# Kernel optimization log

Hardware: AMD Instinct MI355X
Metric: run time of the kernel (lower is better)

## Reference

```python
import jax, jax.numpy as jnp
import numpy as np

EPS = 1e-5

def _layernorm(x, g, b):
    m = jnp.mean(x, axis=-1, keepdims=True)
    v = jnp.mean(jnp.square(x - m), axis=-1, keepdims=True)
    return (x - m) * jax.lax.rsqrt(v + EPS) * g + b

def setup_inputs() -> dict:
    key = jax.random.key(0)
    ks = jax.random.split(key, 4)
    B, N, D = 8, 256, 128
    h = jax.random.normal(ks[0], (B, N, D), dtype=jnp.float32)
    adj_J = jax.random.normal(ks[1], (B, N, N), dtype=jnp.float32)
    W_msg = jax.random.normal(ks[2], (D, 2 * D + 1), dtype=jnp.float32) * 0.05
    W_upd = jax.random.normal(ks[3], (D, 2 * D), dtype=jnp.float32) * 0.05
    return {
        "h": h, "adj_J": adj_J,
        "W_msg": W_msg, "b_msg": jnp.zeros((D,), jnp.float32),
        "g_msg": jnp.ones((D,), jnp.float32), "beta_msg": jnp.zeros((D,), jnp.float32),
        "W_upd": W_upd, "b_upd": jnp.zeros((D,), jnp.float32),
        "g_upd": jnp.ones((D,), jnp.float32), "beta_upd": jnp.zeros((D,), jnp.float32),
    }

def reference(h, adj_J, W_msg, b_msg, g_msg, beta_msg, W_upd, b_upd, g_upd, beta_upd):
    B, N, D = h.shape
    # Split msg Linear weight: cat([h_target, h_source, J]) @ W.T is separable.
    Wt = W_msg[:, :D]        # acts on h_target (node i, dim 1)
    Ws = W_msg[:, D:2 * D]   # acts on h_source (node j, dim 2)
    wJ = W_msg[:, 2 * D]     # acts on scalar J
    # pre[b,i,j,e] = h[b,i]@Wt.T + h[b,j]@Ws.T + J[b,i,j]*wJ + b
    pre = (jnp.einsum('bid,ed->bie', h, Wt)[:, :, None, :]
           + jnp.einsum('bjd,ed->bje', h, Ws)[:, None, :, :]
           + adj_J[..., None] * wJ
           + b_msg)
    messages = jax.nn.silu(_layernorm(pre, g_msg, beta_msg))  # (B,N,N,D)
    # mask out self-messages (j == i) then sum over sources j
    idx = jnp.arange(N)
    agg = jnp.sum(messages, axis=2) - messages[:, idx, idx, :]  # (B,N,D)
    upd_pre = (jnp.einsum('bnd,ed->bne', h, W_upd[:, :D])
               + jnp.einsum('bnd,ed->bne', agg, W_upd[:, D:])
               + b_upd)
    dh = jax.nn.silu(_layernorm(upd_pre, g_upd, beta_upd))
    return h + dh
```

## Files before the change

kernel.cpp:

```cpp
#include <hip/hip_runtime.h>

#define BB 8
#define NN 256
#define DD 128
#define SW 257
#define SU 256
#define EPSV 1e-5f

__device__ __forceinline__ float wave_reduce_add(float v) {
#pragma unroll
  for (int off = 32; off > 0; off >>= 1) v += __shfl_xor(v, off, 64);
  return v;
}

__global__ __launch_bounds__(256) void k_proj(
    const float* __restrict__ h, const float* __restrict__ Wm,
    const float* __restrict__ bmsg,
    float* __restrict__ u, float* __restrict__ s,
    float* __restrict__ rowA, float* __restrict__ rowB,
    float* __restrict__ rowD2, float* __restrict__ rowE2,
    float* __restrict__ wtilv) {
  const int blk = blockIdx.x;
  const int b = blk >> 6;
  const int r0 = (blk & 63) * 4;
  const int tid = threadIdx.x;
  const int half = tid >> 7, e = tid & 127;
  const int wv = tid >> 6, lane = tid & 63;

  __shared__ float hs[4][DD];
  __shared__ float pS[4][4], pw[2], pQ[4][4], pD[4][4];

  const float* hb = h + (size_t)(b * NN + r0) * DD;
  if (tid < DD) {
#pragma unroll
    for (int r = 0; r < 4; ++r) hs[r][e] = hb[r * DD + e];
  }
  __syncthreads();

  float acc[4];
  const float bm = (half == 0) ? bmsg[e] : 0.f;
#pragma unroll
  for (int r = 0; r < 4; ++r) acc[r] = bm;

  const float* wr = Wm + (size_t)e * SW + half * DD;
#pragma unroll 8
  for (int k = 0; k < DD; k += 4) {
    const float4 w4 = *(const float4*)(wr + k);
#pragma unroll
    for (int r = 0; r < 4; ++r) {
      const float4 hv = *(const float4*)(&hs[r][k]);
      acc[r] = fmaf(hv.x, w4.x, acc[r]);
      acc[r] = fmaf(hv.y, w4.y, acc[r]);
      acc[r] = fmaf(hv.z, w4.z, acc[r]);
      acc[r] = fmaf(hv.w, w4.w, acc[r]);
    }
  }

  const float we = Wm[(size_t)e * SW + 2 * DD];
#pragma unroll
  for (int r = 0; r < 4; ++r) {
    const float sm = wave_reduce_add(acc[r]);
    if (lane == 0) pS[wv][r] = sm;
  }
  {
    const float sw = wave_reduce_add(we);
    if (lane == 0 && wv < 2) pw[wv] = sw;
  }
  __syncthreads();

  const int b2 = half * 2;
  const float muw = (pw[0] + pw[1]) * (1.f / DD);
  const float wtil = we - muw;
  float c[4];
#pragma unroll
  for (int r = 0; r < 4; ++r)
    c[r] = acc[r] - (pS[b2][r] + pS[b2 + 1][r]) * (1.f / DD);

  float* outp = (half == 0 ? u : s) + (size_t)(b * NN + r0) * DD;
#pragma unroll
  for (int r = 0; r < 4; ++r) outp[r * DD + e] = c[r];
  if (blk == 0 && half == 0) wtilv[e] = wtil;

#pragma unroll
  for (int r = 0; r < 4; ++r) {
    const float q = wave_reduce_add(c[r] * c[r]);
    const float dd = wave_reduce_add(c[r] * wtil);
    if (lane == 0) { pQ[wv][r] = q; pD[wv][r] = dd; }
  }
  __syncthreads();
  if (tid < 4) {
    const int row = b * NN + r0 + tid;
    rowA[row]  = pQ[0][tid] + pQ[1][tid];
    rowD2[row] = 2.f * (pD[0][tid] + pD[1][tid]);
    rowB[row]  = pQ[2][tid] + pQ[3][tid];
    rowE2[row] = 2.f * (pD[2][tid] + pD[3][tid]);
  }
}

__global__ __launch_bounds__(256) void k_cross(
    const float* __restrict__ u, const float* __restrict__ s,
    const float* __restrict__ rowA, const float* __restrict__ rowB,
    float* __restrict__ Gp) {
  const int bid = blockIdx.x;
  const int b = bid >> 6;
  const int t = bid & 63;
  const int r0 = (t >> 3) * 32, c0 = (t & 7) * 32;
  const int tid = threadIdx.x;
  const int ty = tid >> 4, tx = tid & 15;

  __shared__ float Us[32][132], Ss[32][132];
  const float* ub = u + (size_t)(b * NN + r0) * DD;
  const float* sb = s + (size_t)(b * NN + c0) * DD;
  {
    const int row = tid >> 5, col = (tid & 31) * 4;
#pragma unroll
    for (int rr = 0; rr < 4; ++rr) {
      const float4 uv = *(const float4*)(ub + (size_t)(row + rr * 8) * DD + col);
      const float4 sv = *(const float4*)(sb + (size_t)(row + rr * 8) * DD + col);
      *(float4*)(&Us[row + rr * 8][col]) = uv;
      *(float4*)(&Ss[row + rr * 8][col]) = sv;
    }
  }
  __syncthreads();

  float a00 = 0, a01 = 0, a10 = 0, a11 = 0;
  for (int k = 0; k < DD; k += 4) {
    const float4 A0 = *(const float4*)(&Us[ty][k]);
    const float4 A1 = *(const float4*)(&Us[ty + 16][k]);
    const float4 B0 = *(const float4*)(&Ss[tx][k]);
    const float4 B1 = *(const float4*)(&Ss[tx + 16][k]);
    a00 = fmaf(A0.x, B0.x, a00); a00 = fmaf(A0.y, B0.y, a00);
    a00 = fmaf(A0.z, B0.z, a00); a00 = fmaf(A0.w, B0.w, a00);
    a01 = fmaf(A0.x, B1.x, a01); a01 = fmaf(A0.y, B1.y, a01);
    a01 = fmaf(A0.z, B1.z, a01); a01 = fmaf(A0.w, B1.w, a01);
    a10 = fmaf(A1.x, B0.x, a10); a10 = fmaf(A1.y, B0.y, a10);
    a10 = fmaf(A1.z, B0.z, a10); a10 = fmaf(A1.w, B0.w, a10);
    a11 = fmaf(A1.x, B1.x, a11); a11 = fmaf(A1.y, B1.y, a11);
    a11 = fmaf(A1.z, B1.z, a11); a11 = fmaf(A1.w, B1.w, a11);
  }
  const float Ar0 = rowA[b * NN + r0 + ty];
  const float Ar1 = rowA[b * NN + r0 + ty + 16];
  const float Bc0 = rowB[b * NN + c0 + tx];
  const float Bc1 = rowB[b * NN + c0 + tx + 16];
  float* gp = Gp + ((size_t)(b * NN + r0 + ty)) * NN + c0;
  gp[tx]                = Ar0 + Bc0 + 2.f * a00;
  gp[tx + 16]           = Ar0 + Bc1 + 2.f * a01;
  gp[16 * NN + tx]      = Ar1 + Bc0 + 2.f * a10;
  gp[16 * NN + tx + 16] = Ar1 + Bc1 + 2.f * a11;
}

__global__ __launch_bounds__(256) void k_msg(
    const float* __restrict__ u, const float* __restrict__ s,
    const float* __restrict__ Gp, const float* __restrict__ rowD2,
    const float* __restrict__ rowE2, const float* __restrict__ adj,
    const float* __restrict__ wtilv, const float* __restrict__ g,
    const float* __restrict__ be, float* __restrict__ agg) {
  const int blk = blockIdx.x;
  const int b = blk >> 8, i = blk & 255;
  const int tid = threadIdx.x, lane = tid & 63, wv = tid >> 6;

  __shared__ float4 s_pak[NN];
  __shared__ float sacc[4][DD];

  s_pak[tid] = make_float4(adj[(size_t)blk * NN + tid],
                           Gp[(size_t)blk * NN + tid],
                           rowE2[b * NN + tid], 0.f);

  const float2 uu  = *(const float2*)(u + (size_t)blk * DD + 2 * lane);
  const float2 wt2 = *(const float2*)(wtilv + 2 * lane);
  const float2 g2  = *(const float2*)(g + 2 * lane);
  const float2 be2 = *(const float2*)(be + 2 * lane);
  const float C = wave_reduce_add(fmaf(wt2.x, wt2.x, wt2.y * wt2.y));
  const float D2i = rowD2[blk];
  __syncthreads();

  float acc0 = 0.f, acc1 = 0.f;
  const float* srow = s + (size_t)b * NN * DD + 2 * lane;
#pragma unroll 4
  for (int j = wv; j < NN; j += 4) {
    if (j == i) continue;
    const float4 pk = s_pak[j];
    const float2 ss = *(const float2*)(srow + (size_t)j * DD);
    const float aJ = pk.x;
    const float q = fmaf(aJ, fmaf(aJ, C, D2i + pk.z), pk.y);
    const float rs = __builtin_amdgcn_rsqf(fmaf(q, 1.f / DD, EPSV));
    const float x0 = fmaf(aJ, wt2.x, uu.x + ss.x);
    const float x1 = fmaf(aJ, wt2.y, uu.y + ss.y);
    const float y0 = fmaf(x0 * rs, g2.x, be2.x);
    const float y1 = fmaf(x1 * rs, g2.y, be2.y);
    acc0 = fmaf(y0, __builtin_amdgcn_rcpf(1.f + __expf(-y0)), acc0);
    acc1 = fmaf(y1, __builtin_amdgcn_rcpf(1.f + __expf(-y1)), acc1);
  }
  *(float2*)(&sacc[wv][2 * lane]) = make_float2(acc0, acc1);
  __syncthreads();
  if (tid < DD) {
    agg[(size_t)blk * DD + tid] =
        sacc[0][tid] + sacc[1][tid] + sacc[2][tid] + sacc[3][tid];
  }
}

__global__ __launch_bounds__(256) void k_upd(
    const float* __restrict__ h, const float* __restrict__ agg,
    const float* __restrict__ Wu, const float* __restrict__ bu,
    const float* __restrict__ gu, const float* __restrict__ beu,
    float* __restrict__ out) {
  const int blk = blockIdx.x;
  const int b = blk >> 6;
  const int r0 = (blk & 63) * 4;
  const int tid = threadIdx.x;
  const int half = tid >> 7, e = tid & 127;
  const int wv = tid >> 6, lane = tid & 63;

  __shared__ float hs[4][DD], ags[4][DD], comb[4][DD];
  __shared__ float pm[2][4], pq[2][4];
  const size_t base = (size_t)(b * NN + r0) * DD;
  if (tid < DD) {
#pragma unroll
    for (int r = 0; r < 4; ++r) hs[r][e] = h[base + r * DD + e];
  } else {
#pragma unroll
    for (int r = 0; r < 4; ++r) ags[r][e] = agg[base + r * DD + e];
  }
  __syncthreads();

  float acc[4];
  const float bias = (half == 0) ? bu[e] : 0.f;
#pragma unroll
  for (int r = 0; r < 4; ++r) acc[r] = bias;

  const float* wr = Wu + (size_t)e * SU + half * DD;
  const float(*inp)[DD] = (half == 0) ? hs : ags;
#pragma unroll 8
  for (int k = 0; k < DD; k += 4) {
    const float4 w4 = *(const float4*)(wr + k);
#pragma unroll
    for (int r = 0; r < 4; ++r) {
      const float4 hv = *(const float4*)(&inp[r][k]);
      acc[r] = fmaf(hv.x, w4.x, acc[r]);
      acc[r] = fmaf(hv.y, w4.y, acc[r]);
      acc[r] = fmaf(hv.z, w4.z, acc[r]);
      acc[r] = fmaf(hv.w, w4.w, acc[r]);
    }
  }
  if (half == 1) {
#pragma unroll
    for (int r = 0; r < 4; ++r) comb[r][e] = acc[r];
  }
  __syncthreads();
  float v[4];
  if (half == 0) {
#pragma unroll
    for (int r = 0; r < 4; ++r) {
      v[r] = acc[r] + comb[r][e];
      const float sm = wave_reduce_add(v[r]);
      const float sq = wave_reduce_add(v[r] * v[r]);
      if (lane == 0) { pm[wv][r] = sm; pq[wv][r] = sq; }
    }
  }
  __syncthreads();
  if (half == 0) {
    const float ge = gu[e], bee = beu[e];
#pragma unroll
    for (int r = 0; r < 4; ++r) {
      const float mean = (pm[0][r] + pm[1][r]) * (1.f / DD);
      const float var = (pq[0][r] + pq[1][r]) * (1.f / DD) - mean * mean;
      const float rs = __builtin_amdgcn_rsqf(var + EPSV);
      const float y = fmaf((v[r] - mean) * rs, ge, bee);
      const float sg = __builtin_amdgcn_rcpf(1.f + __expf(-y));
      out[base + r * DD + e] = hs[r][e] + y * sg;
    }
  }
}

extern "C" void kernel_launch(void* const* d_in, const int* in_sizes, int n_in,
                              void* d_out, int out_size, void* d_ws, size_t ws_size,
                              hipStream_t stream) {
  const float* h    = (const float*)d_in[0];
  const float* adj  = (const float*)d_in[1];
  const float* Wm   = (const float*)d_in[2];
  const float* bmsg = (const float*)d_in[3];
  const float* gmsg = (const float*)d_in[4];
  const float* bemsg= (const float*)d_in[5];
  const float* Wu   = (const float*)d_in[6];
  const float* bupd = (const float*)d_in[7];
  const float* gupd = (const float*)d_in[8];
  const float* beupd= (const float*)d_in[9];
  float* out = (float*)d_out;

  float* ws    = (float*)d_ws;
  float* u     = ws;
  float* s     = u + BB * NN * DD;
  float* aggp  = s + BB * NN * DD;
  float* Gp    = aggp + BB * NN * DD;
  float* rowA  = Gp + BB * NN * NN;
  float* rowB  = rowA + BB * NN;
  float* rowD2 = rowB + BB * NN;
  float* rowE2 = rowD2 + BB * NN;
  float* wtilv = rowE2 + BB * NN;

  k_proj<<<512, 256, 0, stream>>>(h, Wm, bmsg, u, s, rowA, rowB, rowD2, rowE2, wtilv);
  k_cross<<<512, 256, 0, stream>>>(u, s, rowA, rowB, Gp);
  k_msg<<<2048, 256, 0, stream>>>(u, s, Gp, rowD2, rowE2, adj, wtilv, gmsg, bemsg, aggp);
  k_upd<<<512, 256, 0, stream>>>(h, aggp, Wu, bupd, gupd, beupd, out);
}
```

Before: 65.46 us.

## Fuse four stage kernels into one cooperative persistent kernel with grid syncs

Replaces the four separate launches (projection, cross Gram, message aggregation, update) with a single cooperative kernel of 1024 blocks that runs each stage in turn, separated by grid-wide syncs. The message stage now has each block handle two rows instead of one row per block. The aim is to remove the launch gaps and tail effects between the four kernels. In exchange it adds three grid barriers and leaves half the blocks idle during three of the stages. It falls back to the old four-kernel path if the occupancy check or the cooperative launch fails.

```diff
diff --git a/kernel.cpp b/kernel.cpp
--- a/kernel.cpp
+++ b/kernel.cpp
@@ -1,4 +1,7 @@
 #include <hip/hip_runtime.h>
+#include <hip/hip_cooperative_groups.h>
+
+namespace cg = cooperative_groups;
 
 #define BB 8
 #define NN 256
@@ -6,11 +9,266 @@
 #define SW 257
 #define SU 256
 #define EPSV 1e-5f
+#define NBF 1024
 
 __device__ __forceinline__ float wave_reduce_add(float v) {
 #pragma unroll
   for (int off = 32; off > 0; off >>= 1) v += __shfl_xor(v, off, 64);
   return v;
+}
+
+__global__ __launch_bounds__(256, 4) void k_fused(
+    const float* __restrict__ h, const float* __restrict__ adj,
+    const float* __restrict__ Wm, const float* __restrict__ bmsg,
+    const float* __restrict__ g, const float* __restrict__ be,
+    const float* __restrict__ Wu, const float* __restrict__ bu,
+    const float* __restrict__ gu, const float* __restrict__ beu,
+    float* __restrict__ out,
+    float* __restrict__ u, float* __restrict__ s, float* __restrict__ aggp,
+    float* __restrict__ Gp, float* __restrict__ rowA, float* __restrict__ rowB,
+    float* __restrict__ rowD2, float* __restrict__ rowE2,
+    float* __restrict__ wtilv) {
+  cg::grid_group grid = cg::this_grid();
+  const int blk = blockIdx.x;
+  const int tid = threadIdx.x;
+  const int lane = tid & 63, wv = tid >> 6;
+
+  __shared__ __align__(16) float smem[2 * 32 * 132];
+  __shared__ float ps_a[4][4], ps_b[4][4], ps_c[4][4], ps_w[2];
+
+  if (blk < 512) {
+    const int b = blk >> 6, r0 = (blk & 63) * 4;
+    const int half = tid >> 7, e = tid & 127;
+    float (*hs)[DD] = (float (*)[DD])smem;
+    const float* hb = h + (size_t)(b * NN + r0) * DD;
+    if (tid < DD) {
+#pragma unroll
+      for (int r = 0; r < 4; ++r) hs[r][e] = hb[r * DD + e];
+    }
+    __syncthreads();
+
+    float acc[4];
+    const float bm = (half == 0) ? bmsg[e] : 0.f;
+#pragma unroll
+    for (int r = 0; r < 4; ++r) acc[r] = bm;
+
+    const float* wr = Wm + (size_t)e * SW + half * DD;
+#pragma unroll 8
+    for (int k = 0; k < DD; k += 4) {
+      const float4 w4 = *(const float4*)(wr + k);
+#pragma unroll
+      for (int r = 0; r < 4; ++r) {
+        const float4 hv = *(const float4*)(&hs[r][k]);
+        acc[r] = fmaf(hv.x, w4.x, acc[r]);
+        acc[r] = fmaf(hv.y, w4.y, acc[r]);
+        acc[r] = fmaf(hv.z, w4.z, acc[r]);
+        acc[r] = fmaf(hv.w, w4.w, acc[r]);
+      }
+    }
+
+    const float we = Wm[(size_t)e * SW + 2 * DD];
+#pragma unroll
+    for (int r = 0; r < 4; ++r) {
+      const float sm = wave_reduce_add(acc[r]);
+      if (lane == 0) ps_a[wv][r] = sm;
+    }
+    {
+      const float sw = wave_reduce_add(we);
+      if (lane == 0 && wv < 2) ps_w[wv] = sw;
+    }
+    __syncthreads();
+
+    const int b2 = half * 2;
+    const float muw = (ps_w[0] + ps_w[1]) * (1.f / DD);
+    const float wtil = we - muw;
+    float c[4];
+#pragma unroll
+    for (int r = 0; r < 4; ++r)
+      c[r] = acc[r] - (ps_a[b2][r] + ps_a[b2 + 1][r]) * (1.f / DD);
+
+    float* outp = (half == 0 ? u : s) + (size_t)(b * NN + r0) * DD;
+#pragma unroll
+    for (int r = 0; r < 4; ++r) outp[r * DD + e] = c[r];
+    if (blk == 0 && half == 0) wtilv[e] = wtil;
+
+#pragma unroll
+    for (int r = 0; r < 4; ++r) {
+      const float q = wave_reduce_add(c[r] * c[r]);
+      const float dd = wave_reduce_add(c[r] * wtil);
+      if (lane == 0) { ps_b[wv][r] = q; ps_c[wv][r] = dd; }
+    }
+    __syncthreads();
+    if (tid < 4) {
+      const int row = b * NN + r0 + tid;
+      rowA[row]  = ps_b[0][tid] + ps_b[1][tid];
+      rowD2[row] = 2.f * (ps_c[0][tid] + ps_c[1][tid]);
+      rowB[row]  = ps_b[2][tid] + ps_b[3][tid];
+      rowE2[row] = 2.f * (ps_c[2][tid] + ps_c[3][tid]);
+    }
+  }
+  grid.sync();
+
+  if (blk < 512) {
+    const int b = blk >> 6;
+    const int t = blk & 63;
+    const int r0 = (t >> 3) * 32, c0 = (t & 7) * 32;
+    const int ty = tid >> 4, tx = tid & 15;
+    float (*Us)[132] = (float (*)[132])smem;
+    float (*Ss)[132] = (float (*)[132])(smem + 32 * 132);
+    const float* ub = u + (size_t)(b * NN + r0) * DD;
+    const float* sb = s + (size_t)(b * NN + c0) * DD;
+    {
+      const int row = tid >> 5, col = (tid & 31) * 4;
+#pragma unroll
+      for (int rr = 0; rr < 4; ++rr) {
+        const float4 uv = *(const float4*)(ub + (size_t)(row + rr * 8) * DD + col);
+        const float4 sv = *(const float4*)(sb + (size_t)(row + rr * 8) * DD + col);
+        *(float4*)(&Us[row + rr * 8][col]) = uv;
+        *(float4*)(&Ss[row + rr * 8][col]) = sv;
+      }
+    }
+    __syncthreads();
+
+    float a00 = 0, a01 = 0, a10 = 0, a11 = 0;
+    for (int k = 0; k < DD; k += 4) {
+      const float4 A0 = *(const float4*)(&Us[ty][k]);
+      const float4 A1 = *(const float4*)(&Us[ty + 16][k]);
+      const float4 B0 = *(const float4*)(&Ss[tx][k]);
+      const float4 B1 = *(const float4*)(&Ss[tx + 16][k]);
+      a00 = fmaf(A0.x, B0.x, a00); a00 = fmaf(A0.y, B0.y, a00);
+      a00 = fmaf(A0.z, B0.z, a00); a00 = fmaf(A0.w, B0.w, a00);
+      a01 = fmaf(A0.x, B1.x, a01); a01 = fmaf(A0.y, B1.y, a01);
+      a01 = fmaf(A0.z, B1.z, a01); a01 = fmaf(A0.w, B1.w, a01);
+      a10 = fmaf(A1.x, B0.x, a10); a10 = fmaf(A1.y, B0.y, a10);
+      a10 = fmaf(A1.z, B0.z, a10); a10 = fmaf(A1.w, B0.w, a10);
+      a11 = fmaf(A1.x, B1.x, a11); a11 = fmaf(A1.y, B1.y, a11);
+      a11 = fmaf(A1.z, B1.z, a11); a11 = fmaf(A1.w, B1.w, a11);
+    }
+    const float Ar0 = rowA[b * NN + r0 + ty];
+    const float Ar1 = rowA[b * NN + r0 + ty + 16];
+    const float Bc0 = rowB[b * NN + c0 + tx];
+    const float Bc1 = rowB[b * NN + c0 + tx + 16];
+    float* gp = Gp + ((size_t)(b * NN + r0 + ty)) * NN + c0;
+    gp[tx]                = Ar0 + Bc0 + 2.f * a00;
+    gp[tx + 16]           = Ar0 + Bc1 + 2.f * a01;
+    gp[16 * NN + tx]      = Ar1 + Bc0 + 2.f * a10;
+    gp[16 * NN + tx + 16] = Ar1 + Bc1 + 2.f * a11;
+  }
+  grid.sync();
+
+  {
+    float4* s_pak = (float4*)smem;
+    float (*sacc)[DD] = (float (*)[DD])(smem + 1024);
+
+    const float2 wt2 = *(const float2*)(wtilv + 2 * lane);
+    const float2 g2  = *(const float2*)(g + 2 * lane);
+    const float2 be2 = *(const float2*)(be + 2 * lane);
+    const float C = wave_reduce_add(fmaf(wt2.x, wt2.x, wt2.y * wt2.y));
+
+#pragma unroll
+    for (int it = 0; it < 2; ++it) {
+      const int idx = blk + it * NBF;
+      const int b = idx >> 8, i = idx & 255;
+
+      s_pak[tid] = make_float4(adj[(size_t)idx * NN + tid],
+                               Gp[(size_t)idx * NN + tid],
+                               rowE2[b * NN + tid], 0.f);
+      const float2 uu = *(const float2*)(u + (size_t)idx * DD + 2 * lane);
+      const float D2i = rowD2[idx];
+      __syncthreads();
+
+      float acc0 = 0.f, acc1 = 0.f;
+      const float* srow = s + (size_t)b * NN * DD + 2 * lane;
+#pragma unroll 4
+      for (int j = wv; j < NN; j += 4) {
+        if (j == i) continue;
+        const float4 pk = s_pak[j];
+        const float2 ss = *(const float2*)(srow + (size_t)j * DD);
+        const float aJ = pk.x;
+        const float q = fmaf(aJ, fmaf(aJ, C, D2i + pk.z), pk.y);
+        const float rs = __builtin_amdgcn_rsqf(fmaf(q, 1.f / DD, EPSV));
+        const float x0 = fmaf(aJ, wt2.x, uu.x + ss.x);
+        const float x1 = fmaf(aJ, wt2.y, uu.y + ss.y);
+        const float y0 = fmaf(x0 * rs, g2.x, be2.x);
+        const float y1 = fmaf(x1 * rs, g2.y, be2.y);
+        acc0 = fmaf(y0, __builtin_amdgcn_rcpf(1.f + __expf(-y0)), acc0);
+        acc1 = fmaf(y1, __builtin_amdgcn_rcpf(1.f + __expf(-y1)), acc1);
+      }
+      *(float2*)(&sacc[wv][2 * lane]) = make_float2(acc0, acc1);
+      __syncthreads();
+      if (tid < DD) {
+        aggp[(size_t)idx * DD + tid] =
+            sacc[0][tid] + sacc[1][tid] + sacc[2][tid] + sacc[3][tid];
+      }
+      __syncthreads();
+    }
+  }
+  grid.sync();
+
+  if (blk < 512) {
+    const int b = blk >> 6, r0 = (blk & 63) * 4;
+    const int half = tid >> 7, e = tid & 127;
+    float (*hs)[DD]   = (float (*)[DD])smem;
+    float (*ags)[DD]  = (float (*)[DD])(smem + 512);
+    float (*comb)[DD] = (float (*)[DD])(smem + 1024);
+    const size_t base = (size_t)(b * NN + r0) * DD;
+    if (tid < DD) {
+#pragma unroll
+      for (int r = 0; r < 4; ++r) hs[r][e] = h[base + r * DD + e];
+    } else {
+#pragma unroll
+      for (int r = 0; r < 4; ++r) ags[r][e] = aggp[base + r * DD + e];
+    }
+    __syncthreads();
+
+    float acc[4];
+    const float bias = (half == 0) ? bu[e] : 0.f;
+#pragma unroll
+    for (int r = 0; r < 4; ++r) acc[r] = bias;
+
+    const float* wr = Wu + (size_t)e * SU + half * DD;
+    const float(*inp)[DD] = (half == 0) ? hs : ags;
+#pragma unroll 8
+    for (int k = 0; k < DD; k += 4) {
+      const float4 w4 = *(const float4*)(wr + k);
+#pragma unroll
+      for (int r = 0; r < 4; ++r) {
+        const float4 hv = *(const float4*)(&inp[r][k]);
+        acc[r] = fmaf(hv.x, w4.x, acc[r]);
+        acc[r] = fmaf(hv.y, w4.y, acc[r]);
+        acc[r] = fmaf(hv.z, w4.z, acc[r]);
+        acc[r] = fmaf(hv.w, w4.w, acc[r]);
+      }
+    }
+    if (half == 1) {
+#pragma unroll
+      for (int r = 0; r < 4; ++r) comb[r][e] = acc[r];
+    }
+    __syncthreads();
+    float v[4];
+    if (half == 0) {
+#pragma unroll
+      for (int r = 0; r < 4; ++r) {
+        v[r] = acc[r] + comb[r][e];
+        const float sm = wave_reduce_add(v[r]);
+        const float sq = wave_reduce_add(v[r] * v[r]);
+        if (lane == 0) { ps_a[wv][r] = sm; ps_b[wv][r] = sq; }
+      }
+    }
+    __syncthreads();
+    if (half == 0) {
+      const float ge = gu[e], bee = beu[e];
+#pragma unroll
+      for (int r = 0; r < 4; ++r) {
+        const float mean = (ps_a[0][r] + ps_a[1][r]) * (1.f / DD);
+        const float var = (ps_b[0][r] + ps_b[1][r]) * (1.f / DD) - mean * mean;
+        const float rs = __builtin_amdgcn_rsqf(var + EPSV);
+        const float y = fmaf((v[r] - mean) * rs, ge, bee);
+        const float sg = __builtin_amdgcn_rcpf(1.f + __expf(-y));
+        out[base + r * DD + e] = hs[r][e] + y * sg;
+      }
+    }
+  }
 }
 
 __global__ __launch_bounds__(256) void k_proj(
@@ -298,6 +556,21 @@
   float* rowE2 = rowD2 + BB * NN;
   float* wtilv = rowE2 + BB * NN;
 
+  int maxBlocksPerCU = 0;
+  hipError_t qe = hipOccupancyMaxActiveBlocksPerMultiprocessor(
+      &maxBlocksPerCU, (const void*)k_fused, 256, 0);
+  if (qe == hipSuccess && maxBlocksPerCU >= 4) {
+    void* args[] = {(void*)&h,    (void*)&adj,  (void*)&Wm,    (void*)&bmsg,
+                    (void*)&gmsg, (void*)&bemsg,(void*)&Wu,    (void*)&bupd,
+                    (void*)&gupd, (void*)&beupd,(void*)&out,   (void*)&u,
+                    (void*)&s,    (void*)&aggp, (void*)&Gp,    (void*)&rowA,
+                    (void*)&rowB, (void*)&rowD2,(void*)&rowE2, (void*)&wtilv};
+    hipError_t le = hipLaunchCooperativeKernel((const void*)k_fused,
+                                               dim3(NBF), dim3(256), args, 0,
+                                               stream);
+    if (le == hipSuccess) return;
+  }
+
   k_proj<<<512, 256, 0, stream>>>(h, Wm, bmsg, u, s, rowA, rowB, rowD2, rowE2, wtilv);
   k_cross<<<512, 256, 0, stream>>>(u, s, rowA, rowB, Gp);
   k_msg<<<2048, 256, 0, stream>>>(u, s, Gp, rowD2, rowE2, adj, wtilv, gmsg, bemsg, aggp);
```

Result: no change. 66.28 us (+1.3%).

## Fuse cross-term, message aggregation and update into one kernel over row pairs

Applied to the files above, without the earlier changes.

Replaces the k_cross, k_msg and k_upd kernels with a single kernel that handles two target rows per block. It tiles s through shared memory, computes the u·s dot products on the fly instead of materializing the Gp matrix, aggregates messages, and then applies the update linear, layernorm and SiLU in place. k_proj now also writes a transposed copy of W_upd so the fused update reads weights coalesced. This removes two kernel launches and the global round trips for Gp and agg, but each block now reloads all of s for only two rows and has less parallelism per block.

```diff
diff --git a/kernel.cpp b/kernel.cpp
--- a/kernel.cpp
+++ b/kernel.cpp
@@ -15,11 +15,11 @@
 
 __global__ __launch_bounds__(256) void k_proj(
     const float* __restrict__ h, const float* __restrict__ Wm,
-    const float* __restrict__ bmsg,
+    const float* __restrict__ bmsg, const float* __restrict__ Wu,
     float* __restrict__ u, float* __restrict__ s,
     float* __restrict__ rowA, float* __restrict__ rowB,
     float* __restrict__ rowD2, float* __restrict__ rowE2,
-    float* __restrict__ wtilv) {
+    float* __restrict__ wtilv, float* __restrict__ wut) {
   const int blk = blockIdx.x;
   const int b = blk >> 6;
   const int r0 = (blk & 63) * 4;
@@ -35,6 +35,11 @@
 #pragma unroll
     for (int r = 0; r < 4; ++r) hs[r][e] = hb[r * DD + e];
   }
+  if (tid >= DD && tid < DD + 64) {
+    const int i = blk * 64 + (tid - DD);
+    const int d = i >> 7, e2 = i & 127;
+    wut[i] = Wu[(size_t)e2 * SU + d];
+  }
   __syncthreads();
 
   float acc[4];
@@ -97,177 +102,170 @@
   }
 }
 
-__global__ __launch_bounds__(256) void k_cross(
-    const float* __restrict__ u, const float* __restrict__ s,
+__global__ __launch_bounds__(256) void k_msgfused(
+    const float* __restrict__ h, const float* __restrict__ u,
+    const float* __restrict__ s, const float* __restrict__ adj,
     const float* __restrict__ rowA, const float* __restrict__ rowB,
-    float* __restrict__ Gp) {
-  const int bid = blockIdx.x;
-  const int b = bid >> 6;
-  const int t = bid & 63;
-  const int r0 = (t >> 3) * 32, c0 = (t & 7) * 32;
-  const int tid = threadIdx.x;
-  const int ty = tid >> 4, tx = tid & 15;
-
-  __shared__ float Us[32][132], Ss[32][132];
-  const float* ub = u + (size_t)(b * NN + r0) * DD;
-  const float* sb = s + (size_t)(b * NN + c0) * DD;
+    const float* __restrict__ rowD2, const float* __restrict__ rowE2,
+    const float* __restrict__ wtilv, const float* __restrict__ g,
+    const float* __restrict__ be, const float* __restrict__ wut,
+    const float* __restrict__ bu, const float* __restrict__ gu,
+    const float* __restrict__ beu, float* __restrict__ out) {
+  const int blk = blockIdx.x;
+  const int b = blk >> 7, ip = blk & 127;
+  const int i0 = 2 * ip, i1 = i0 + 1;
+  const int tid = threadIdx.x, lane = tid & 63, wv = tid >> 6;
+  const int bNN = b * NN;
+
+  __shared__ __align__(16) float st_[32 * 132];
+  __shared__ __align__(16) float upair_[2 * DD];
+  __shared__ __align__(16) float hrow_[2 * DD];
+  __shared__ float2 pak0[32], pak1[32];
+  __shared__ float pm[2][2], pq[2][2];
+
   {
-    const int row = tid >> 5, col = (tid & 31) * 4;
-#pragma unroll
-    for (int rr = 0; rr < 4; ++rr) {
-      const float4 uv = *(const float4*)(ub + (size_t)(row + rr * 8) * DD + col);
-      const float4 sv = *(const float4*)(sb + (size_t)(row + rr * 8) * DD + col);
-      *(float4*)(&Us[row + rr * 8][col]) = uv;
-      *(float4*)(&Ss[row + rr * 8][col]) = sv;
-    }
-  }
-  __syncthreads();
-
-  float a00 = 0, a01 = 0, a10 = 0, a11 = 0;
-  for (int k = 0; k < DD; k += 4) {
-    const float4 A0 = *(const float4*)(&Us[ty][k]);
-    const float4 A1 = *(const float4*)(&Us[ty + 16][k]);
-    const float4 B0 = *(const float4*)(&Ss[tx][k]);
-    const float4 B1 = *(const float4*)(&Ss[tx + 16][k]);
-    a00 = fmaf(A0.x, B0.x, a00); a00 = fmaf(A0.y, B0.y, a00);
-    a00 = fmaf(A0.z, B0.z, a00); a00 = fmaf(A0.w, B0.w, a00);
-    a01 = fmaf(A0.x, B1.x, a01); a01 = fmaf(A0.y, B1.y, a01);
-    a01 = fmaf(A0.z, B1.z, a01); a01 = fmaf(A0.w, B1.w, a01);
-    a10 = fmaf(A1.x, B0.x, a10); a10 = fmaf(A1.y, B0.y, a10);
-    a10 = fmaf(A1.z, B0.z, a10); a10 = fmaf(A1.w, B0.w, a10);
-    a11 = fmaf(A1.x, B1.x, a11); a11 = fmaf(A1.y, B1.y, a11);
-    a11 = fmaf(A1.z, B1.z, a11); a11 = fmaf(A1.w, B1.w, a11);
-  }
-  const float Ar0 = rowA[b * NN + r0 + ty];
-  const float Ar1 = rowA[b * NN + r0 + ty + 16];
-  const float Bc0 = rowB[b * NN + c0 + tx];
-  const float Bc1 = rowB[b * NN + c0 + tx + 16];
-  float* gp = Gp + ((size_t)(b * NN + r0 + ty)) * NN + c0;
-  gp[tx]                = Ar0 + Bc0 + 2.f * a00;
-  gp[tx + 16]           = Ar0 + Bc1 + 2.f * a01;
-  gp[16 * NN + tx]      = Ar1 + Bc0 + 2.f * a10;
-  gp[16 * NN + tx + 16] = Ar1 + Bc1 + 2.f * a11;
-}
-
-__global__ __launch_bounds__(256) void k_msg(
-    const float* __restrict__ u, const float* __restrict__ s,
-    const float* __restrict__ Gp, const float* __restrict__ rowD2,
-    const float* __restrict__ rowE2, const float* __restrict__ adj,
-    const float* __restrict__ wtilv, const float* __restrict__ g,
-    const float* __restrict__ be, float* __restrict__ agg) {
-  const int blk = blockIdx.x;
-  const int b = blk >> 8, i = blk & 255;
-  const int tid = threadIdx.x, lane = tid & 63, wv = tid >> 6;
-
-  __shared__ float4 s_pak[NN];
-  __shared__ float sacc[4][DD];
-
-  s_pak[tid] = make_float4(adj[(size_t)blk * NN + tid],
-                           Gp[(size_t)blk * NN + tid],
-                           rowE2[b * NN + tid], 0.f);
-
-  const float2 uu  = *(const float2*)(u + (size_t)blk * DD + 2 * lane);
+    const int ii = tid >> 7, e = tid & 127;
+    upair_[ii * DD + e] = u[(size_t)(bNN + i0 + ii) * DD + e];
+    hrow_[ii * DD + e]  = h[(size_t)(bNN + i0 + ii) * DD + e];
+  }
   const float2 wt2 = *(const float2*)(wtilv + 2 * lane);
   const float2 g2  = *(const float2*)(g + 2 * lane);
   const float2 be2 = *(const float2*)(be + 2 * lane);
   const float C = wave_reduce_add(fmaf(wt2.x, wt2.x, wt2.y * wt2.y));
-  const float D2i = rowD2[blk];
-  __syncthreads();
-
-  float acc0 = 0.f, acc1 = 0.f;
-  const float* srow = s + (size_t)b * NN * DD + 2 * lane;
-#pragma unroll 4
-  for (int j = wv; j < NN; j += 4) {
-    if (j == i) continue;
-    const float4 pk = s_pak[j];
-    const float2 ss = *(const float2*)(srow + (size_t)j * DD);
-    const float aJ = pk.x;
-    const float q = fmaf(aJ, fmaf(aJ, C, D2i + pk.z), pk.y);
-    const float rs = __builtin_amdgcn_rsqf(fmaf(q, 1.f / DD, EPSV));
-    const float x0 = fmaf(aJ, wt2.x, uu.x + ss.x);
-    const float x1 = fmaf(aJ, wt2.y, uu.y + ss.y);
-    const float y0 = fmaf(x0 * rs, g2.x, be2.x);
-    const float y1 = fmaf(x1 * rs, g2.y, be2.y);
-    acc0 = fmaf(y0, __builtin_amdgcn_rcpf(1.f + __expf(-y0)), acc0);
-    acc1 = fmaf(y1, __builtin_amdgcn_rcpf(1.f + __expf(-y1)), acc1);
-  }
-  *(float2*)(&sacc[wv][2 * lane]) = make_float2(acc0, acc1);
-  __syncthreads();
-  if (tid < DD) {
-    agg[(size_t)blk * DD + tid] =
-        sacc[0][tid] + sacc[1][tid] + sacc[2][tid] + sacc[3][tid];
-  }
-}
-
-__global__ __launch_bounds__(256) void k_upd(
-    const float* __restrict__ h, const float* __restrict__ agg,
-    const float* __restrict__ Wu, const float* __restrict__ bu,
-    const float* __restrict__ gu, const float* __restrict__ beu,
-    float* __restrict__ out) {
-  const int blk = blockIdx.x;
-  const int b = blk >> 6;
-  const int r0 = (blk & 63) * 4;
-  const int tid = threadIdx.x;
+  const float A0 = rowA[bNN + i0], A1 = rowA[bNN + i1];
+  const float D20 = rowD2[bNN + i0], D21 = rowD2[bNN + i1];
+  __syncthreads();
+  const float2 uu0 = *(const float2*)(&upair_[2 * lane]);
+  const float2 uu1 = *(const float2*)(&upair_[DD + 2 * lane]);
+
+  float accA0 = 0.f, accA1 = 0.f, accB0 = 0.f, accB1 = 0.f;
+  const float* sb = s + (size_t)bNN * DD;
+
+  for (int tile = 0; tile < 8; ++tile) {
+    const int t0 = tile * 32;
+    __syncthreads();
+    {
+      const int r = tid >> 5, c4 = (tid & 31) * 4;
+#pragma unroll
+      for (int p = 0; p < 4; ++p) {
+        const int row = p * 8 + r;
+        *(float4*)(&st_[row * 132 + c4]) =
+            *(const float4*)(sb + (size_t)(t0 + row) * DD + c4);
+      }
+    }
+    __syncthreads();
+    {
+      const int j = tid >> 3, seg = tid & 7, k0 = seg * 16;
+      float d0 = 0.f, d1 = 0.f;
+#pragma unroll
+      for (int k = 0; k < 16; k += 4) {
+        const float4 sv = *(const float4*)(&st_[j * 132 + k0 + k]);
+        const float4 u0v = *(const float4*)(&upair_[k0 + k]);
+        const float4 u1v = *(const float4*)(&upair_[DD + k0 + k]);
+        d0 = fmaf(sv.x, u0v.x, d0); d0 = fmaf(sv.y, u0v.y, d0);
+        d0 = fmaf(sv.z, u0v.z, d0); d0 = fmaf(sv.w, u0v.w, d0);
+        d1 = fmaf(sv.x, u1v.x, d1); d1 = fmaf(sv.y, u1v.y, d1);
+        d1 = fmaf(sv.z, u1v.z, d1); d1 = fmaf(sv.w, u1v.w, d1);
+      }
+#pragma unroll
+      for (int m = 1; m < 8; m <<= 1) {
+        d0 += __shfl_xor(d0, m, 64);
+        d1 += __shfl_xor(d1, m, 64);
+      }
+      if (seg == 0) {
+        const int jg = t0 + j;
+        const float Bj = rowB[bNN + jg], E2j = rowE2[bNN + jg];
+        const float a0 = adj[(size_t)(bNN + i0) * NN + jg];
+        const float a1 = adj[(size_t)(bNN + i1) * NN + jg];
+        const float q0 = fmaf(a0, fmaf(a0, C, D20 + E2j), A0 + Bj + 2.f * d0);
+        const float q1 = fmaf(a1, fmaf(a1, C, D21 + E2j), A1 + Bj + 2.f * d1);
+        pak0[j] = make_float2(a0, __builtin_amdgcn_rsqf(fmaf(q0, 1.f / DD, EPSV)));
+        pak1[j] = make_float2(a1, __builtin_amdgcn_rsqf(fmaf(q1, 1.f / DD, EPSV)));
+      }
+    }
+    __syncthreads();
+    for (int jj = wv; jj < 32; jj += 4) {
+      const int jg = t0 + jj;
+      const float2 ss = *(const float2*)(&st_[jj * 132 + 2 * lane]);
+      const float sx0 = uu0.x + ss.x, sx1 = uu0.y + ss.y;
+      const float tx0 = uu1.x + ss.x, tx1 = uu1.y + ss.y;
+      if (jg != i0) {
+        const float2 p = pak0[jj];
+        const float x0 = fmaf(p.x, wt2.x, sx0);
+        const float x1 = fmaf(p.x, wt2.y, sx1);
+        const float y0 = fmaf(x0 * p.y, g2.x, be2.x);
+        const float y1 = fmaf(x1 * p.y, g2.y, be2.y);
+        accA0 = fmaf(y0, __builtin_amdgcn_rcpf(1.f + __expf(-y0)), accA0);
+        accA1 = fmaf(y1, __builtin_amdgcn_rcpf(1.f + __expf(-y1)), accA1);
+      }
+      if (jg != i1) {
+        const float2 p = pak1[jj];
+        const float x0 = fmaf(p.x, wt2.x, tx0);
+        const float x1 = fmaf(p.x, wt2.y, tx1);
+        const float y0 = fmaf(x0 * p.y, g2.x, be2.x);
+        const float y1 = fmaf(x1 * p.y, g2.y, be2.y);
+        accB0 = fmaf(y0, __builtin_amdgcn_rcpf(1.f + __expf(-y0)), accB0);
+        accB1 = fmaf(y1, __builtin_amdgcn_rcpf(1.f + __expf(-y1)), accB1);
+      }
+    }
+  }
+
+  __syncthreads();
+  *(float2*)(&st_[(wv * 2 + 0) * DD + 2 * lane]) = make_float2(accA0, accA1);
+  *(float2*)(&st_[(wv * 2 + 1) * DD + 2 * lane]) = make_float2(accB0, accB1);
+  __syncthreads();
+  {
+    const int ii = tid >> 7, e = tid & 127;
+    st_[(8 + ii) * DD + e] = st_[(0 * 2 + ii) * DD + e] +
+                             st_[(1 * 2 + ii) * DD + e] +
+                             st_[(2 * 2 + ii) * DD + e] +
+                             st_[(3 * 2 + ii) * DD + e];
+  }
+  __syncthreads();
+
   const int half = tid >> 7, e = tid & 127;
-  const int wv = tid >> 6, lane = tid & 63;
-
-  __shared__ float hs[4][DD], ags[4][DD], comb[4][DD];
-  __shared__ float pm[2][4], pq[2][4];
-  const size_t base = (size_t)(b * NN + r0) * DD;
-  if (tid < DD) {
-#pragma unroll
-    for (int r = 0; r < 4; ++r) hs[r][e] = h[base + r * DD + e];
-  } else {
-#pragma unroll
-    for (int r = 0; r < 4; ++r) ags[r][e] = agg[base + r * DD + e];
-  }
-  __syncthreads();
-
-  float acc[4];
-  const float bias = (half == 0) ? bu[e] : 0.f;
-#pragma unroll
-  for (int r = 0; r < 4; ++r) acc[r] = bias;
-
-  const float* wr = Wu + (size_t)e * SU + half * DD;
-  const float(*inp)[DD] = (half == 0) ? hs : ags;
+  float v0 = (half == 0) ? bu[e] : 0.f;
+  float v1 = v0;
+  {
+    const float* xin = (half == 0) ? hrow_ : &st_[8 * DD];
+    const float* wcol = wut + (size_t)half * DD * DD + e;
 #pragma unroll 8
-  for (int k = 0; k < DD; k += 4) {
-    const float4 w4 = *(const float4*)(wr + k);
-#pragma unroll
-    for (int r = 0; r < 4; ++r) {
-      const float4 hv = *(const float4*)(&inp[r][k]);
-      acc[r] = fmaf(hv.x, w4.x, acc[r]);
-      acc[r] = fmaf(hv.y, w4.y, acc[r]);
-      acc[r] = fmaf(hv.z, w4.z, acc[r]);
-      acc[r] = fmaf(hv.w, w4.w, acc[r]);
-    }
-  }
-  if (half == 1) {
-#pragma unroll
-    for (int r = 0; r < 4; ++r) comb[r][e] = acc[r];
-  }
-  __syncthreads();
-  float v[4];
+    for (int k = 0; k < DD; ++k) {
+      const float w = wcol[(size_t)k * DD];
+      v0 = fmaf(xin[k], w, v0);
+      v1 = fmaf(xin[DD + k], w, v1);
+    }
+  }
+  if (half == 1) { upair_[e] = v0; upair_[DD + e] = v1; }
+  __syncthreads();
   if (half == 0) {
-#pragma unroll
-    for (int r = 0; r < 4; ++r) {
-      v[r] = acc[r] + comb[r][e];
-      const float sm = wave_reduce_add(v[r]);
-      const float sq = wave_reduce_add(v[r] * v[r]);
-      if (lane == 0) { pm[wv][r] = sm; pq[wv][r] = sq; }
+    v0 += upair_[e];
+    v1 += upair_[DD + e];
+    const float sm0 = wave_reduce_add(v0), sq0 = wave_reduce_add(v0 * v0);
+    const float sm1 = wave_reduce_add(v1), sq1 = wave_reduce_add(v1 * v1);
+    if (lane == 0) {
+      pm[wv][0] = sm0; pq[wv][0] = sq0;
+      pm[wv][1] = sm1; pq[wv][1] = sq1;
     }
   }
   __syncthreads();
   if (half == 0) {
     const float ge = gu[e], bee = beu[e];
-#pragma unroll
-    for (int r = 0; r < 4; ++r) {
-      const float mean = (pm[0][r] + pm[1][r]) * (1.f / DD);
-      const float var = (pq[0][r] + pq[1][r]) * (1.f / DD) - mean * mean;
+    {
+      const float mean = (pm[0][0] + pm[1][0]) * (1.f / DD);
+      const float var = (pq[0][0] + pq[1][0]) * (1.f / DD) - mean * mean;
       const float rs = __builtin_amdgcn_rsqf(var + EPSV);
-      const float y = fmaf((v[r] - mean) * rs, ge, bee);
+      const float y = fmaf((v0 - mean) * rs, ge, bee);
       const float sg = __builtin_amdgcn_rcpf(1.f + __expf(-y));
-      out[base + r * DD + e] = hs[r][e] + y * sg;
+      out[(size_t)(bNN + i0) * DD + e] = hrow_[e] + y * sg;
+    }
+    {
+      const float mean = (pm[0][1] + pm[1][1]) * (1.f / DD);
+      const float var = (pq[0][1] + pq[1][1]) * (1.f / DD) - mean * mean;
+      const float rs = __builtin_amdgcn_rsqf(var + EPSV);
+      const float y = fmaf((v1 - mean) * rs, ge, bee);
+      const float sg = __builtin_amdgcn_rcpf(1.f + __expf(-y));
+      out[(size_t)(bNN + i1) * DD + e] = hrow_[DD + e] + y * sg;
     }
   }
 }
@@ -290,16 +288,16 @@
   float* ws    = (float*)d_ws;
   float* u     = ws;
   float* s     = u + BB * NN * DD;
-  float* aggp  = s + BB * NN * DD;
-  float* Gp    = aggp + BB * NN * DD;
-  float* rowA  = Gp + BB * NN * NN;
+  float* rowA  = s + BB * NN * DD;
   float* rowB  = rowA + BB * NN;
   float* rowD2 = rowB + BB * NN;
   float* rowE2 = rowD2 + BB * NN;
   float* wtilv = rowE2 + BB * NN;
-
-  k_proj<<<512, 256, 0, stream>>>(h, Wm, bmsg, u, s, rowA, rowB, rowD2, rowE2, wtilv);
-  k_cross<<<512, 256, 0, stream>>>(u, s, rowA, rowB, Gp);
-  k_msg<<<2048, 256, 0, stream>>>(u, s, Gp, rowD2, rowE2, adj, wtilv, gmsg, bemsg, aggp);
-  k_upd<<<512, 256, 0, stream>>>(h, aggp, Wu, bupd, gupd, beupd, out);
+  float* wut   = wtilv + DD;
+
+  k_proj<<<512, 256, 0, stream>>>(h, Wm, bmsg, Wu, u, s, rowA, rowB, rowD2,
+                                  rowE2, wtilv, wut);
+  k_msgfused<<<1024, 256, 0, stream>>>(h, u, s, adj, rowA, rowB, rowD2, rowE2,
+                                       wtilv, gmsg, bemsg, wut, bupd, gupd,
+                                       beupd, out);
 }
```

After: 56.30 us. -14.0%, faster.
